# Performance work log

Measured on AMD Instinct MI355X. Metric: run time of the kernel, lower is better.

Reference implementation:

```python
import jax, jax.numpy as jnp
import numpy as np

SOS = 1  # letter2index['<sos>']
EOS = 0  # letter2index['<eos>'] (embedding padding_idx)

B, T, KV, E, H, V, L = 64, 2048, 128, 256, 512, 30, 256


def _lstm_cell(x, h, c, W_ih, W_hh, b_ih, b_hh):
    # PyTorch LSTMCell: gates ordered (i, f, g, o)
    gates = x @ W_ih.T + b_ih + h @ W_hh.T + b_hh
    i, f, g, o = jnp.split(gates, 4, axis=-1)
    c_new = jax.nn.sigmoid(f) * c + jax.nn.sigmoid(i) * jnp.tanh(g)
    h_new = jax.nn.sigmoid(o) * jnp.tanh(c_new)
    return h_new, c_new


def setup_inputs() -> dict:
    root = jax.random.key(0)
    ks = jax.random.split(root, 16)

    key = jax.random.normal(ks[0], (B, T, KV), dtype=jnp.float32)
    value = jax.random.normal(ks[1], (B, T, KV), dtype=jnp.float32)
    encoder_len = jax.random.randint(ks[2], (B,), 1, T + 1)
    y = jax.random.randint(ks[3], (B, L), 0, V)

    def w(k, shape, fan_in):
        return jax.random.normal(k, shape, dtype=jnp.float32) / np.sqrt(fan_in)

    emb_weight = w(ks[4], (V, E), E).at[EOS].set(0.0)  # padding_idx row zeroed
    in1 = E + KV
    W_ih1 = w(ks[5], (4 * H, in1), in1)
    W_hh1 = w(ks[6], (4 * H, H), H)
    b_ih1 = jnp.zeros((4 * H,), jnp.float32)
    b_hh1 = jnp.zeros((4 * H,), jnp.float32)
    W_ih2 = w(ks[7], (4 * KV, H), H)
    W_hh2 = w(ks[8], (4 * KV, KV), KV)
    b_ih2 = jnp.zeros((4 * KV,), jnp.float32)
    b_hh2 = jnp.zeros((4 * KV,), jnp.float32)
    out_bias = jnp.zeros((V,), jnp.float32)

    return dict(key=key, value=value, encoder_len=encoder_len, y=y,
                emb_weight=emb_weight,
                W_ih1=W_ih1, W_hh1=W_hh1, b_ih1=b_ih1, b_hh1=b_hh1,
                W_ih2=W_ih2, W_hh2=W_hh2, b_ih2=b_ih2, b_hh2=b_hh2,
                out_bias=out_bias)


def reference(key, value, encoder_len, y, emb_weight,
              W_ih1, W_hh1, b_ih1, b_hh1,
              W_ih2, W_hh2, b_ih2, b_hh2, out_bias):
    Bq, Tq, d_k = key.shape
    mask = jnp.arange(Tq)[None, :] >= encoder_len[:, None]  # (B, T) True = padded
    scale = 1.0 / np.sqrt(d_k).astype(np.float32)

    # Teacher forcing rate 1.0 in train mode: step i uses embed(SOS) at i=0,
    # embed(y[:, i-1]) afterwards.
    ids = jnp.concatenate([jnp.full((Bq, 1), SOS, dtype=y.dtype), y[:, :-1]], axis=1)
    embeds = emb_weight[ids]               # (B, L, E)
    embeds_t = jnp.swapaxes(embeds, 0, 1)  # (L, B, E)

    h_dim = W_hh1.shape[1]
    kv_dim = W_hh2.shape[1]
    init = (jnp.zeros((Bq, h_dim), key.dtype), jnp.zeros((Bq, h_dim), key.dtype),
            jnp.zeros((Bq, kv_dim), key.dtype), jnp.zeros((Bq, kv_dim), key.dtype),
            value.mean(axis=1))  # initial context

    def step(carry, char_embed):
        h1, c1, h2, c2, context = carry
        x = jnp.concatenate([char_embed, context], axis=1)
        h1, c1 = _lstm_cell(x, h1, c1, W_ih1, W_hh1, b_ih1, b_hh1)
        h2, c2 = _lstm_cell(h1, h2, c2, W_ih2, W_hh2, b_ih2, b_hh2)
        query = h2                                             # (B, KV)
        energy = jnp.einsum('bd,btd->bt', query, key) * scale  # (B, T)
        energy = jnp.where(mask, -1e9, energy)
        attn = jax.nn.softmax(energy, axis=1)
        ctx = jnp.einsum('bt,btd->bd', attn, value)            # (B, KV)
        logits = jnp.concatenate([query, ctx], axis=1) @ emb_weight.T + out_bias
        return (h1, c1, h2, c2, ctx), (logits, attn[0])

    _, (preds, attn_plot) = jax.lax.scan(step, init, embeds_t)
    predictions = jnp.swapaxes(preds, 0, 1)  # (B, L, V)
    return predictions, attn_plot            # attn_plot: (L, T), batch element 0
```

## Files before the change

### kernel.cpp

```cpp
#include <hip/hip_runtime.h>

#define NB 256
#define NT 1024

#define BB   64
#define TTS  2048
#define DKV  128
#define EEM  256
#define HH1  512
#define VVV  30
#define LLS  256
#define SOS_ID 1
#define SCALE_F 0.088388347648318447f

#define OFF_PM    0
#define OFF_PS    256
#define OFF_PCTX  512
#define OFF_WSE   33280
#define OFF_EMBT  35328
#define OFF_H1    68096
#define OFF_C1    133632
#define OFF_H2R   166400
#define OFF_H2T   182784
#define OFF_C2    199168
#define OFF_BAR   207360
#define OFF_KBF   212992
#define OFF_VBF   8601600
#define WS_NEED_BYTES 67960832ull
#define PRED_SZ   491520

struct Params {
  const float* key; const float* value;
  const int* enc_len; const int* y;
  const float* emb;
  const float* Wih1; const float* Whh1; const float* bih1; const float* bhh1;
  const float* Wih2; const float* Whh2; const float* bih2; const float* bhh2;
  const float* obias;
  float* out; float* ws;
};

struct SMEM {
  union {
    struct {
      float ctxT[8192];
      union { float wt[8192]; float red[8192]; } u;
    } a;
    struct { float wm[16]; float wS[16]; float wctx[2048]; } c;
  };
};

__device__ __forceinline__ float sigm(float x) { return 1.f / (1.f + __expf(-x)); }
__device__ __forceinline__ float tanh_f(float x) {
  float t = __expf(-2.f * fabsf(x));
  float r = (1.f - t) / (1.f + t);
  return x < 0.f ? -r : r;
}
__device__ __forceinline__ unsigned bfr(float f) {
  unsigned u = __float_as_uint(f);
  return (u + 0x7FFFu + ((u >> 16) & 1u)) >> 16;
}
__device__ __forceinline__ float b2f(unsigned short h) {
  return __uint_as_float(((unsigned)h) << 16);
}
__device__ __forceinline__ float blo(unsigned u) { return __uint_as_float(u << 16); }
__device__ __forceinline__ float bhi(unsigned u) { return __uint_as_float(u & 0xffff0000u); }

__device__ __forceinline__ void gbar(unsigned* base) {
  __syncthreads();
  if (threadIdx.x == 0) {
    __builtin_amdgcn_fence(__ATOMIC_RELEASE, "agent");
    unsigned* gen = base + 1056;
    unsigned g = __hip_atomic_load(gen, __ATOMIC_RELAXED, __HIP_MEMORY_SCOPE_AGENT);
    unsigned* gcnt = base + (blockIdx.x & 31) * 32;
    if (__hip_atomic_fetch_add(gcnt, 1u, __ATOMIC_RELAXED, __HIP_MEMORY_SCOPE_AGENT) == 7u) {
      unsigned* mcnt = base + 1024;
      if (__hip_atomic_fetch_add(mcnt, 1u, __ATOMIC_RELAXED, __HIP_MEMORY_SCOPE_AGENT) == 31u) {
        #pragma unroll
        for (int gg = 0; gg < 32; ++gg)
          __hip_atomic_store(base + gg * 32, 0u, __ATOMIC_RELAXED, __HIP_MEMORY_SCOPE_AGENT);
        __hip_atomic_store(mcnt, 0u, __ATOMIC_RELAXED, __HIP_MEMORY_SCOPE_AGENT);
        __hip_atomic_store(gen, g + 1u, __ATOMIC_RELEASE, __HIP_MEMORY_SCOPE_AGENT);
      }
    }
    int guard = 0;
    while (__hip_atomic_load(gen, __ATOMIC_RELAXED, __HIP_MEMORY_SCOPE_AGENT) == g) {
      __builtin_amdgcn_s_sleep(2);
      if (++guard > 50000000) break;
    }
    __builtin_amdgcn_fence(__ATOMIC_ACQUIRE, "agent");
  }
  __syncthreads();
}

__device__ __forceinline__ void mac8x4(float acc[8][4], const float* wt, int k, float4 x4) {
  float4 wa = *(const float4*)(wt + k*8);
  float4 wb = *(const float4*)(wt + k*8 + 4);
  float wr[8] = {wa.x, wa.y, wa.z, wa.w, wb.x, wb.y, wb.z, wb.w};
  float xr[4] = {x4.x, x4.y, x4.z, x4.w};
  #pragma unroll
  for (int r = 0; r < 8; ++r)
    #pragma unroll
    for (int c = 0; c < 4; ++c)
      acc[r][c] += wr[r] * xr[c];
}

__device__ __forceinline__ void gate_reduce_store(float acc[8][4], float* red, int tid) {
  #pragma unroll
  for (int r = 0; r < 8; ++r) {
    #pragma unroll
    for (int c = 0; c < 4; ++c) {
      float v = acc[r][c];
      v += __shfl_xor(v, 16);
      v += __shfl_xor(v, 32);
      acc[r][c] = v;
    }
  }
  int wv = tid >> 6, b0 = tid & 15;
  if ((tid & 63) < 16) {
    #pragma unroll
    for (int r = 0; r < 8; ++r)
      *(float4*)(red + wv*512 + r*64 + b0*4) =
        make_float4(acc[r][0], acc[r][1], acc[r][2], acc[r][3]);
  }
}

template<bool MEAN, bool BF16>
__device__ void phase_attn(const Params& p, const float* qrow,
                           const unsigned short* kbf, const unsigned short* vbf,
                           float* pm, float* pS, float* pctx, float* wsE,
                           SMEM* sm, int bj, int tid) {
  const int lane = tid & 63, w = tid >> 6;
  const int b = bj >> 2, s = bj & 3;
  const int len = MEAN ? TTS : p.enc_len[b];
  const int sub = lane & 15, grp = lane >> 4;
  const int q = 4*w + s;
  const int r0 = q*4 + grp;
  float m = -1e30f, S = 0.f;
  float ca[8] = {0.f,0.f,0.f,0.f,0.f,0.f,0.f,0.f};
  if constexpr (MEAN) {
    const float* vb = p.value + (size_t)b * TTS * DKV;
    #pragma unroll
    for (int j = 0; j < 8; ++j) {
      int t = r0 + 256*j;
      const float* vp = vb + (size_t)t * DKV + sub*8;
      float4 va = *(const float4*)vp;
      float4 vb4 = *(const float4*)(vp + 4);
      S += 1.f;
      ca[0]+=va.x;  ca[1]+=va.y;  ca[2]+=va.z;  ca[3]+=va.w;
      ca[4]+=vb4.x; ca[5]+=vb4.y; ca[6]+=vb4.z; ca[7]+=vb4.w;
    }
    m = 0.f;
  } else {
    int NJ = 0;
    if (len > q*4) { int nj = (len - q*4 + 255) >> 8; NJ = nj < 8 ? nj : 8; }
    if (NJ > 0) {
      float q8[8];
      {
        const float* qp = qrow + b*DKV + sub*8;
        float4 qa = *(const float4*)qp;
        float4 qb = *(const float4*)(qp + 4);
        q8[0]=qa.x; q8[1]=qa.y; q8[2]=qa.z; q8[3]=qa.w;
        q8[4]=qb.x; q8[5]=qb.y; q8[6]=qb.z; q8[7]=qb.w;
      }
      float e[8];
      #pragma unroll
      for (int j = 0; j < 8; ++j) e[j] = -1e30f;
      if constexpr (BF16) {
        const unsigned short* kb  = kbf + (size_t)(b*TTS)*DKV + sub*8;
        const unsigned short* vbp = vbf + (size_t)(b*TTS)*DKV + sub*8;
        uint4 kq[8], vq[8];
        #pragma unroll
        for (int j = 0; j < 8; ++j) {
          if (j < NJ) {
            int t = r0 + 256*j;
            int tc = t < len ? t : len - 1;
            kq[j] = *(const uint4*)(kb  + (size_t)tc * DKV);
            vq[j] = *(const uint4*)(vbp + (size_t)tc * DKV);
          }
        }
        __builtin_amdgcn_sched_barrier(0);
        #pragma unroll
        for (int j = 0; j < 8; ++j) {
          if (j < NJ) {
            float ep = blo(kq[j].x)*q8[0] + bhi(kq[j].x)*q8[1]
                     + blo(kq[j].y)*q8[2] + bhi(kq[j].y)*q8[3]
                     + blo(kq[j].z)*q8[4] + bhi(kq[j].z)*q8[5]
                     + blo(kq[j].w)*q8[6] + bhi(kq[j].w)*q8[7];
            ep += __shfl_xor(ep, 1); ep += __shfl_xor(ep, 2);
            ep += __shfl_xor(ep, 4); ep += __shfl_xor(ep, 8);
            int t = r0 + 256*j;
            e[j] = (t < len) ? ep * SCALE_F : -1e30f;
            if (b == 0 && sub == 0 && t < len) wsE[t] = e[j];
          }
        }
        m = fmaxf(fmaxf(fmaxf(e[0],e[1]), fmaxf(e[2],e[3])),
                  fmaxf(fmaxf(e[4],e[5]), fmaxf(e[6],e[7])));
        float pr[8];
        #pragma unroll
        for (int j = 0; j < 8; ++j) {
          pr[j] = (e[j] > -1e29f) ? __expf(e[j] - m) : 0.f;
          S += pr[j];
        }
        #pragma unroll
        for (int j = 0; j < 8; ++j) {
          if (j < NJ) {
            ca[0] += pr[j]*blo(vq[j].x); ca[1] += pr[j]*bhi(vq[j].x);
            ca[2] += pr[j]*blo(vq[j].y); ca[3] += pr[j]*bhi(vq[j].y);
            ca[4] += pr[j]*blo(vq[j].z); ca[5] += pr[j]*bhi(vq[j].z);
            ca[6] += pr[j]*blo(vq[j].w); ca[7] += pr[j]*bhi(vq[j].w);
          }
        }
      } else {
        #pragma unroll
        for (int j = 0; j < 8; ++j) {
          if (j < NJ) {
            int t = r0 + 256*j;
            int tc = t < len ? t : len - 1;
            const float* kp = p.key + (size_t)(b*TTS + tc)*DKV + sub*8;
            float4 ka = *(const float4*)kp;
            float4 kb2 = *(const float4*)(kp + 4);
            float ep = ka.x*q8[0] + ka.y*q8[1] + ka.z*q8[2] + ka.w*q8[3]
                     + kb2.x*q8[4] + kb2.y*q8[5] + kb2.z*q8[6] + kb2.w*q8[7];
            ep += __shfl_xor(ep, 1); ep += __shfl_xor(ep, 2);
            ep += __shfl_xor(ep, 4); ep += __shfl_xor(ep, 8);
            e[j] = (t < len) ? ep * SCALE_F : -1e30f;
            if (b == 0 && sub == 0 && t < len) wsE[t] = e[j];
          }
        }
        m = fmaxf(fmaxf(fmaxf(e[0],e[1]), fmaxf(e[2],e[3])),
                  fmaxf(fmaxf(e[4],e[5]), fmaxf(e[6],e[7])));
        float pr[8];
        #pragma unroll
        for (int j = 0; j < 8; ++j) {
          pr[j] = (e[j] > -1e29f) ? __expf(e[j] - m) : 0.f;
          S += pr[j];
        }
        #pragma unroll
        for (int j = 0; j < 8; ++j) {
          if (j < NJ) {
            int t = r0 + 256*j;
            int tc = t < len ? t : len - 1;
            const float* vp = p.value + (size_t)(b*TTS + tc)*DKV + sub*8;
            float4 va = *(const float4*)vp;
            float4 vb4 = *(const float4*)(vp + 4);
            ca[0] += pr[j]*va.x;  ca[1] += pr[j]*va.y;
            ca[2] += pr[j]*va.z;  ca[3] += pr[j]*va.w;
            ca[4] += pr[j]*vb4.x; ca[5] += pr[j]*vb4.y;
            ca[6] += pr[j]*vb4.z; ca[7] += pr[j]*vb4.w;
          }
        }
      }
    }
  }
  #pragma unroll
  for (int off = 16; off <= 32; off <<= 1) {
    float mo = __shfl_xor(m, off);
    float So = __shfl_xor(S, off);
    float M2 = fmaxf(m, mo);
    float a0 = __expf(m - M2), a1 = __expf(mo - M2);
    S = S*a0 + So*a1;
    #pragma unroll
    for (int d = 0; d < 8; ++d)
      ca[d] = ca[d]*a0 + __shfl_xor(ca[d], off)*a1;
    m = M2;
  }
  if (lane == 0) { sm->c.wm[w] = m; sm->c.wS[w] = S; }
  if (grp == 0) {
    *(float4*)(sm->c.wctx + w*DKV + sub*8)     = make_float4(ca[0],ca[1],ca[2],ca[3]);
    *(float4*)(sm->c.wctx + w*DKV + sub*8 + 4) = make_float4(ca[4],ca[5],ca[6],ca[7]);
  }
  __syncthreads();
  if (tid < DKV) {
    int d = tid;
    float M = -1e30f;
    #pragma unroll
    for (int ww = 0; ww < 16; ++ww) M = fmaxf(M, sm->c.wm[ww]);
    float Z = 0.f, acc2 = 0.f;
    #pragma unroll
    for (int ww = 0; ww < 16; ++ww) {
      float aw = __expf(sm->c.wm[ww] - M);
      Z += aw * sm->c.wS[ww];
      acc2 += aw * sm->c.wctx[ww*DKV + d];
    }
    pctx[d*256 + b*4 + s] = acc2;
    if (d == 0) { pm[b*4 + s] = M; pS[b*4 + s] = Z; }
  }
}

template<bool BF16>
__global__ void __launch_bounds__(NT, 4) decoder_kernel(Params p) {
  const int tid = threadIdx.x;
  const int bj = blockIdx.x;
  float* ws = p.ws;
  unsigned* bar = (unsigned*)(ws + OFF_BAR);
  float* pm = ws + OFF_PM;
  float* pS = ws + OFF_PS;
  float* pctx = ws + OFF_PCTX;
  float* wsE = ws + OFF_WSE;
  float* embT0 = ws + OFF_EMBT;
  float* embT1 = ws + OFF_EMBT + EEM*BB;
  float* h1b0 = ws + OFF_H1;
  float* h1b1 = ws + OFF_H1 + HH1*BB;
  float* c1 = ws + OFF_C1;
  float* h2r0 = ws + OFF_H2R;
  float* h2r1 = ws + OFF_H2R + BB*DKV;
  float* h2t0 = ws + OFF_H2T;
  float* h2t1 = ws + OFF_H2T + DKV*BB;
  float* c2 = ws + OFF_C2;
  unsigned short* kbf = (unsigned short*)(ws + OFF_KBF);
  unsigned short* vbf = (unsigned short*)(ws + OFF_VBF);

  __shared__ SMEM sm;

  float wr1[8] = {0,0,0,0,0,0,0,0};
  if (tid < 896) {
    #pragma unroll
    for (int r = 0; r < 8; ++r) {
      int grow = (r >> 1)*HH1 + 2*bj + (r & 1);
      wr1[r] = (tid < 384) ? p.Wih1[(size_t)grow*384 + tid]
                           : p.Whh1[(size_t)grow*HH1 + (tid - 384)];
    }
  }
  float wr2[8] = {0,0,0,0,0,0,0,0};
  if (bj < 64 && tid < 640) {
    #pragma unroll
    for (int r = 0; r < 8; ++r) {
      int grow = (r >> 1)*DKV + 2*bj + (r & 1);
      wr2[r] = (tid < 512) ? p.Wih2[(size_t)grow*HH1 + tid]
                           : p.Whh2[(size_t)grow*DKV + (tid - 512)];
    }
  }
  float bsum1 = 0.f, bsum2 = 0.f;
  if (tid < 512) {
    int r = tid >> 6;
    int g1 = (r >> 1)*HH1 + 2*bj + (r & 1);
    bsum1 = p.bih1[g1] + p.bhh1[g1];
    if (bj < 64) {
      int g2 = (r >> 1)*DKV + 2*bj + (r & 1);
      bsum2 = p.bih2[g2] + p.bhh2[g2];
    }
  }

  {
    int gid = bj*NT + tid;
    for (int idx = gid; idx < (OFF_BAR - OFF_H1); idx += NB*NT) ws[OFF_H1 + idx] = 0.f;
    for (int idx = gid; idx < EEM*BB; idx += NB*NT) {
      int k = idx >> 6, b = idx & 63;
      embT0[k*64 + b] = p.emb[SOS_ID*EEM + k];
    }
    if constexpr (BF16) {
      const int NG = (BB*TTS*DKV) / 8;
      for (int g = gid; g < NG; g += NB*NT) {
        const float4* src = (const float4*)p.key + (size_t)g*2;
        float4 a = src[0], bq = src[1];
        uint4 o;
        o.x = bfr(a.x)  | (bfr(a.y)  << 16);
        o.y = bfr(a.z)  | (bfr(a.w)  << 16);
        o.z = bfr(bq.x) | (bfr(bq.y) << 16);
        o.w = bfr(bq.z) | (bfr(bq.w) << 16);
        ((uint4*)kbf)[g] = o;
      }
      for (int g = gid; g < NG; g += NB*NT) {
        const float4* src = (const float4*)p.value + (size_t)g*2;
        float4 a = src[0], bq = src[1];
        uint4 o;
        o.x = bfr(a.x)  | (bfr(a.y)  << 16);
        o.y = bfr(a.z)  | (bfr(a.w)  << 16);
        o.z = bfr(bq.x) | (bfr(bq.y) << 16);
        o.w = bfr(bq.z) | (bfr(bq.w) << 16);
        ((uint4*)vbf)[g] = o;
      }
    }
    phase_attn<true, BF16>(p, nullptr, kbf, vbf, pm, pS, pctx, wsE, &sm, bj, tid);
  }
  gbar(bar);

  for (int i = 0; i <= LLS; ++i) {
    const int cur = i & 1;
    float* h1c = cur ? h1b1 : h1b0;
    const float* h1p = cur ? h1b0 : h1b1;
    float* h2rc = cur ? h2r1 : h2r0;
    const float* h2rp = cur ? h2r0 : h2r1;
    float* h2tc = cur ? h2t1 : h2t0;
    const float* h2tp = cur ? h2t0 : h2t1;
    const float* et = cur ? embT1 : embT0;
    float* etn = cur ? embT0 : embT1;

    {
      int b = tid & 63, dg = tid >> 6;
      float4 m4 = *(const float4*)(pm + b*4);
      float4 s4 = *(const float4*)(pS + b*4);
      float M = fmaxf(fmaxf(m4.x, m4.y), fmaxf(m4.z, m4.w));
      float a0 = __expf(m4.x - M), a1 = __expf(m4.y - M);
      float a2 = __expf(m4.z - M), a3 = __expf(m4.w - M);
      float Z = a0*s4.x + a1*s4.y + a2*s4.z + a3*s4.w;
      float iZ = 1.f / Z;
      a0 *= iZ; a1 *= iZ; a2 *= iZ; a3 *= iZ;
      #pragma unroll
      for (int jj = 0; jj < 8; ++jj) {
        int d = dg + jj*16;
        float4 c4 = *(const float4*)(pctx + d*256 + b*4);
        sm.a.ctxT[d*64 + b] = a0*c4.x + a1*c4.y + a2*c4.z + a3*c4.w;
      }
    }
    if (i < LLS && tid < 896) {
      *(float4*)(sm.a.u.wt + tid*8)     = make_float4(wr1[0], wr1[1], wr1[2], wr1[3]);
      *(float4*)(sm.a.u.wt + tid*8 + 4) = make_float4(wr1[4], wr1[5], wr1[6], wr1[7]);
    }
    __syncthreads();

    if (i < LLS) {
      {
        const int b0 = tid & 15, ks = tid >> 4;
        float acc[8][4];
        #pragma unroll
        for (int r = 0; r < 8; ++r) { acc[r][0]=0.f; acc[r][1]=0.f; acc[r][2]=0.f; acc[r][3]=0.f; }
        #pragma unroll
        for (int j = 0; j < 4; ++j) {
          int k = ks*4 + j;
          float4 x4 = *(const float4*)(et + k*64 + b0*4);
          mac8x4(acc, sm.a.u.wt, k, x4);
        }
        #pragma unroll
        for (int j = 0; j < 2; ++j) {
          int d = ks*2 + j;
          float4 x4 = *(const float4*)(sm.a.ctxT + d*64 + b0*4);
          mac8x4(acc, sm.a.u.wt, 256 + d, x4);
        }
        #pragma unroll
        for (int j = 0; j < 8; ++j) {
          int kk = ks*8 + j;
          float4 x4 = *(const float4*)(h1p + kk*64 + b0*4);
          mac8x4(acc, sm.a.u.wt, 384 + kk, x4);
        }
        __syncthreads();
        gate_reduce_store(acc, sm.a.u.red, tid);
      }
      __syncthreads();
      if (tid < 512) {
        int r = tid >> 6, b = tid & 63;
        float s = 0.f;
        #pragma unroll
        for (int w2 = 0; w2 < 16; ++w2) s += sm.a.u.red[w2*512 + r*64 + b];
        s += bsum1;
        sm.a.u.red[r*64 + b] = s;
      }
      __syncthreads();
      if (tid < 128) {
        int hh = tid >> 6, b = tid & 63;
        int h = 2*bj + hh;
        float gi = sm.a.u.red[(hh+0)*64 + b];
        float gf = sm.a.u.red[(hh+2)*64 + b];
        float gg = sm.a.u.red[(hh+4)*64 + b];
        float go = sm.a.u.red[(hh+6)*64 + b];
        float co = c1[h*64 + b];
        float cn = sigm(gf)*co + sigm(gi)*tanh_f(gg);
        float hn = sigm(go)*tanh_f(cn);
        c1[h*64 + b] = cn;
        h1c[h*64 + b] = hn;
      }
    }

    if (i >= 1) {
      if (tid >= 960) {
        int ln = tid - 960;
        int oi = bj*8 + (ln >> 3);
        int sub = ln & 7;
        if (oi < BB*VVV) {
          int b = oi / VVV, v = oi - b*VVV;
          float a = 0.f;
          if (sub < 4) {
            #pragma unroll 8
            for (int e0 = 0; e0 < 32; ++e0) {
              int e = sub*32 + e0;
              a += h2rp[b*DKV + e] * p.emb[v*EEM + e];
            }
          } else {
            #pragma unroll 8
            for (int e0 = 0; e0 < 32; ++e0) {
              int d = (sub - 4)*32 + e0;
              a += sm.a.ctxT[d*64 + b] * p.emb[v*EEM + 128 + d];
            }
          }
          a += __shfl_xor(a, 1); a += __shfl_xor(a, 2); a += __shfl_xor(a, 4);
          if (sub == 0) p.out[((size_t)b*LLS + (i-1))*VVV + v] = a + p.obias[v];
        }
      }
      if (tid >= 896 && tid < 904) {
        int t = bj*8 + (tid - 896);
        int len0 = p.enc_len[0];
        float v = 0.f;
        if (t < len0) {
          float m0 = pm[0], m1 = pm[1], m2 = pm[2], m3 = pm[3];
          float M = fmaxf(fmaxf(m0, m1), fmaxf(m2, m3));
          float Z = __expf(m0 - M)*pS[0] + __expf(m1 - M)*pS[1]
                  + __expf(m2 - M)*pS[2] + __expf(m3 - M)*pS[3];
          v = __expf(wsE[t] - M) / Z;
        }
        p.out[PRED_SZ + (size_t)(i-1)*TTS + t] = v;
      }
    }

    if (i == LLS) break;
    gbar(bar);

    if (bj < 64) {
      if (tid < 640) {
        *(float4*)(sm.a.u.wt + tid*8)     = make_float4(wr2[0], wr2[1], wr2[2], wr2[3]);
        *(float4*)(sm.a.u.wt + tid*8 + 4) = make_float4(wr2[4], wr2[5], wr2[6], wr2[7]);
      }
      __syncthreads();
      {
        const int b0 = tid & 15, ks = tid >> 4;
        float acc[8][4];
        #pragma unroll
        for (int r = 0; r < 8; ++r) { acc[r][0]=0.f; acc[r][1]=0.f; acc[r][2]=0.f; acc[r][3]=0.f; }
        #pragma unroll
        for (int j = 0; j < 8; ++j) {
          int k = ks*8 + j;
          float4 x4 = *(const float4*)(h1c + k*64 + b0*4);
          mac8x4(acc, sm.a.u.wt, k, x4);
        }
        #pragma unroll
        for (int j = 0; j < 2; ++j) {
          int d = ks*2 + j;
          float4 x4 = *(const float4*)(h2tp + d*64 + b0*4);
          mac8x4(acc, sm.a.u.wt, 512 + d, x4);
        }
        __syncthreads();
        gate_reduce_store(acc, sm.a.u.red, tid);
      }
      __syncthreads();
      if (tid < 512) {
        int r = tid >> 6, b = tid & 63;
        float s = 0.f;
        #pragma unroll
        for (int w2 = 0; w2 < 16; ++w2) s += sm.a.u.red[w2*512 + r*64 + b];
        s += bsum2;
        sm.a.u.red[r*64 + b] = s;
      }
      __syncthreads();
      if (tid < 128) {
        int hh = tid >> 6, b = tid & 63;
        int d2 = 2*bj + hh;
        float gi = sm.a.u.red[(hh+0)*64 + b];
        float gf = sm.a.u.red[(hh+2)*64 + b];
        float gg = sm.a.u.red[(hh+4)*64 + b];
        float go = sm.a.u.red[(hh+6)*64 + b];
        float co = c2[d2*64 + b];
        float cn = sigm(gf)*co + sigm(gi)*tanh_f(gg);
        float hn = sigm(go)*tanh_f(cn);
        c2[d2*64 + b] = cn;
        h2rc[b*DKV + d2] = hn;
        h2tc[d2*64 + b] = hn;
      }
    } else if (bj < 128) {
      int sn = i + 1;
      if (sn < LLS && tid < 256) {
        int idx = (bj - 64)*256 + tid;
        int k = idx >> 6, b = idx & 63;
        int id = p.y[b*LLS + sn - 1];
        etn[k*64 + b] = p.emb[(size_t)id*EEM + k];
      }
    }
    gbar(bar);

    phase_attn<false, BF16>(p, h2rc, kbf, vbf, pm, pS, pctx, wsE, &sm, bj, tid);
    gbar(bar);
  }
}

__global__ void init_bar_kernel(unsigned* bar) {
  int i = blockIdx.x * blockDim.x + threadIdx.x;
  if (i < 2048) bar[i] = 0u;
}

extern "C" void kernel_launch(void* const* d_in, const int* in_sizes, int n_in,
                              void* d_out, int out_size, void* d_ws, size_t ws_size,
                              hipStream_t stream) {
  Params prm;
  prm.key     = (const float*)d_in[0];
  prm.value   = (const float*)d_in[1];
  prm.enc_len = (const int*)d_in[2];
  prm.y       = (const int*)d_in[3];
  prm.emb     = (const float*)d_in[4];
  prm.Wih1    = (const float*)d_in[5];
  prm.Whh1    = (const float*)d_in[6];
  prm.bih1    = (const float*)d_in[7];
  prm.bhh1    = (const float*)d_in[8];
  prm.Wih2    = (const float*)d_in[9];
  prm.Whh2    = (const float*)d_in[10];
  prm.bih2    = (const float*)d_in[11];
  prm.bhh2    = (const float*)d_in[12];
  prm.obias   = (const float*)d_in[13];
  prm.out = (float*)d_out;
  prm.ws  = (float*)d_ws;

  unsigned* bar = (unsigned*)((float*)d_ws + OFF_BAR);
  init_bar_kernel<<<8, 256, 0, stream>>>(bar);

  void* args[] = { &prm };
  if (ws_size >= WS_NEED_BYTES) {
    hipError_t e = hipLaunchCooperativeKernel((const void*)decoder_kernel<true>,
                                              dim3(NB), dim3(NT), args, 0, stream);
    if (e != hipSuccess) decoder_kernel<true><<<dim3(NB), dim3(NT), 0, stream>>>(prm);
  } else {
    hipError_t e = hipLaunchCooperativeKernel((const void*)decoder_kernel<false>,
                                              dim3(NB), dim3(NT), args, 0, stream);
    if (e != hipSuccess) decoder_kernel<false><<<dim3(NB), dim3(NT), 0, stream>>>(prm);
  }
}
```

Baseline: 17.20 ms.

## Use per-group generation flags in grid barrier and remap attention block assignment

The grid barrier now has each group of eight blocks spin on its own generation flag, which is a monotonically increasing expected counter, instead of all blocks polling one shared word. The aim is to reduce contention on a single cache line. The attention phase remaps block-to-batch assignment so that consecutive blocks handle different batch rows, which spreads variable-length work across groups. It also splits the bf16 key and value loads into two batches to reduce register pressure. Barrier storage grows and the sleep interval is longer, which may add wake-up latency.

```diff
diff --git a/kernel.cpp b/kernel.cpp
--- a/kernel.cpp
+++ b/kernel.cpp
@@ -65,27 +65,30 @@
 __device__ __forceinline__ float blo(unsigned u) { return __uint_as_float(u << 16); }
 __device__ __forceinline__ float bhi(unsigned u) { return __uint_as_float(u & 0xffff0000u); }
 
-__device__ __forceinline__ void gbar(unsigned* base) {
+__device__ __forceinline__ void gbar(unsigned* base, unsigned expect) {
   __syncthreads();
   if (threadIdx.x == 0) {
     __builtin_amdgcn_fence(__ATOMIC_RELEASE, "agent");
-    unsigned* gen = base + 1056;
-    unsigned g = __hip_atomic_load(gen, __ATOMIC_RELAXED, __HIP_MEMORY_SCOPE_AGENT);
-    unsigned* gcnt = base + (blockIdx.x & 31) * 32;
+    const int grp = blockIdx.x >> 3;
+    unsigned* gcnt = base + grp * 32;
     if (__hip_atomic_fetch_add(gcnt, 1u, __ATOMIC_RELAXED, __HIP_MEMORY_SCOPE_AGENT) == 7u) {
       unsigned* mcnt = base + 1024;
       if (__hip_atomic_fetch_add(mcnt, 1u, __ATOMIC_RELAXED, __HIP_MEMORY_SCOPE_AGENT) == 31u) {
+        __hip_atomic_store(mcnt, 0u, __ATOMIC_RELAXED, __HIP_MEMORY_SCOPE_AGENT);
         #pragma unroll
         for (int gg = 0; gg < 32; ++gg)
           __hip_atomic_store(base + gg * 32, 0u, __ATOMIC_RELAXED, __HIP_MEMORY_SCOPE_AGENT);
-        __hip_atomic_store(mcnt, 0u, __ATOMIC_RELAXED, __HIP_MEMORY_SCOPE_AGENT);
-        __hip_atomic_store(gen, g + 1u, __ATOMIC_RELEASE, __HIP_MEMORY_SCOPE_AGENT);
-      }
-    }
+        __builtin_amdgcn_fence(__ATOMIC_RELEASE, "agent");
+        #pragma unroll
+        for (int gg = 0; gg < 32; ++gg)
+          __hip_atomic_store(base + 2048 + gg * 32, expect, __ATOMIC_RELAXED, __HIP_MEMORY_SCOPE_AGENT);
+      }
+    }
+    unsigned* mygen = base + 2048 + grp * 32;
     int guard = 0;
-    while (__hip_atomic_load(gen, __ATOMIC_RELAXED, __HIP_MEMORY_SCOPE_AGENT) == g) {
-      __builtin_amdgcn_s_sleep(2);
-      if (++guard > 50000000) break;
+    while ((int)(__hip_atomic_load(mygen, __ATOMIC_RELAXED, __HIP_MEMORY_SCOPE_AGENT) - expect) < 0) {
+      __builtin_amdgcn_s_sleep(8);
+      if (++guard > 10000000) break;
     }
     __builtin_amdgcn_fence(__ATOMIC_ACQUIRE, "agent");
   }
@@ -130,7 +133,8 @@
                            float* pm, float* pS, float* pctx, float* wsE,
                            SMEM* sm, int bj, int tid) {
   const int lane = tid & 63, w = tid >> 6;
-  const int b = bj >> 2, s = bj & 3;
+  const int b = ((bj & 7) << 3) | ((bj >> 3) & 7);
+  const int s = bj >> 6;
   const int len = MEAN ? TTS : p.enc_len[b];
   const int sub = lane & 15, grp = lane >> 4;
   const int q = 4*w + s;
@@ -150,105 +154,97 @@
       ca[4]+=vb4.x; ca[5]+=vb4.y; ca[6]+=vb4.z; ca[7]+=vb4.w;
     }
     m = 0.f;
-  } else {
-    int NJ = 0;
-    if (len > q*4) { int nj = (len - q*4 + 255) >> 8; NJ = nj < 8 ? nj : 8; }
-    if (NJ > 0) {
-      float q8[8];
-      {
-        const float* qp = qrow + b*DKV + sub*8;
-        float4 qa = *(const float4*)qp;
-        float4 qb = *(const float4*)(qp + 4);
-        q8[0]=qa.x; q8[1]=qa.y; q8[2]=qa.z; q8[3]=qa.w;
-        q8[4]=qb.x; q8[5]=qb.y; q8[6]=qb.z; q8[7]=qb.w;
-      }
-      float e[8];
-      #pragma unroll
-      for (int j = 0; j < 8; ++j) e[j] = -1e30f;
-      if constexpr (BF16) {
-        const unsigned short* kb  = kbf + (size_t)(b*TTS)*DKV + sub*8;
-        const unsigned short* vbp = vbf + (size_t)(b*TTS)*DKV + sub*8;
-        uint4 kq[8], vq[8];
-        #pragma unroll
-        for (int j = 0; j < 8; ++j) {
-          if (j < NJ) {
-            int t = r0 + 256*j;
-            int tc = t < len ? t : len - 1;
-            kq[j] = *(const uint4*)(kb  + (size_t)tc * DKV);
-            vq[j] = *(const uint4*)(vbp + (size_t)tc * DKV);
-          }
-        }
-        __builtin_amdgcn_sched_barrier(0);
-        #pragma unroll
-        for (int j = 0; j < 8; ++j) {
-          if (j < NJ) {
-            float ep = blo(kq[j].x)*q8[0] + bhi(kq[j].x)*q8[1]
-                     + blo(kq[j].y)*q8[2] + bhi(kq[j].y)*q8[3]
-                     + blo(kq[j].z)*q8[4] + bhi(kq[j].z)*q8[5]
-                     + blo(kq[j].w)*q8[6] + bhi(kq[j].w)*q8[7];
-            ep += __shfl_xor(ep, 1); ep += __shfl_xor(ep, 2);
-            ep += __shfl_xor(ep, 4); ep += __shfl_xor(ep, 8);
-            int t = r0 + 256*j;
-            e[j] = (t < len) ? ep * SCALE_F : -1e30f;
-            if (b == 0 && sub == 0 && t < len) wsE[t] = e[j];
-          }
-        }
-        m = fmaxf(fmaxf(fmaxf(e[0],e[1]), fmaxf(e[2],e[3])),
-                  fmaxf(fmaxf(e[4],e[5]), fmaxf(e[6],e[7])));
-        float pr[8];
-        #pragma unroll
-        for (int j = 0; j < 8; ++j) {
-          pr[j] = (e[j] > -1e29f) ? __expf(e[j] - m) : 0.f;
-          S += pr[j];
-        }
-        #pragma unroll
-        for (int j = 0; j < 8; ++j) {
-          if (j < NJ) {
-            ca[0] += pr[j]*blo(vq[j].x); ca[1] += pr[j]*bhi(vq[j].x);
-            ca[2] += pr[j]*blo(vq[j].y); ca[3] += pr[j]*bhi(vq[j].y);
-            ca[4] += pr[j]*blo(vq[j].z); ca[5] += pr[j]*bhi(vq[j].z);
-            ca[6] += pr[j]*blo(vq[j].w); ca[7] += pr[j]*bhi(vq[j].w);
-          }
-        }
-      } else {
-        #pragma unroll
-        for (int j = 0; j < 8; ++j) {
-          if (j < NJ) {
-            int t = r0 + 256*j;
-            int tc = t < len ? t : len - 1;
-            const float* kp = p.key + (size_t)(b*TTS + tc)*DKV + sub*8;
-            float4 ka = *(const float4*)kp;
-            float4 kb2 = *(const float4*)(kp + 4);
-            float ep = ka.x*q8[0] + ka.y*q8[1] + ka.z*q8[2] + ka.w*q8[3]
-                     + kb2.x*q8[4] + kb2.y*q8[5] + kb2.z*q8[6] + kb2.w*q8[7];
-            ep += __shfl_xor(ep, 1); ep += __shfl_xor(ep, 2);
-            ep += __shfl_xor(ep, 4); ep += __shfl_xor(ep, 8);
-            e[j] = (t < len) ? ep * SCALE_F : -1e30f;
-            if (b == 0 && sub == 0 && t < len) wsE[t] = e[j];
-          }
-        }
-        m = fmaxf(fmaxf(fmaxf(e[0],e[1]), fmaxf(e[2],e[3])),
-                  fmaxf(fmaxf(e[4],e[5]), fmaxf(e[6],e[7])));
-        float pr[8];
-        #pragma unroll
-        for (int j = 0; j < 8; ++j) {
-          pr[j] = (e[j] > -1e29f) ? __expf(e[j] - m) : 0.f;
-          S += pr[j];
-        }
-        #pragma unroll
-        for (int j = 0; j < 8; ++j) {
-          if (j < NJ) {
-            int t = r0 + 256*j;
-            int tc = t < len ? t : len - 1;
-            const float* vp = p.value + (size_t)(b*TTS + tc)*DKV + sub*8;
-            float4 va = *(const float4*)vp;
-            float4 vb4 = *(const float4*)(vp + 4);
-            ca[0] += pr[j]*va.x;  ca[1] += pr[j]*va.y;
-            ca[2] += pr[j]*va.z;  ca[3] += pr[j]*va.w;
-            ca[4] += pr[j]*vb4.x; ca[5] += pr[j]*vb4.y;
-            ca[6] += pr[j]*vb4.z; ca[7] += pr[j]*vb4.w;
-          }
-        }
+  } else if (len > q*4) {
+    float q8[8];
+    {
+      const float* qp = qrow + b*DKV + sub*8;
+      float4 qa = *(const float4*)qp;
+      float4 qb = *(const float4*)(qp + 4);
+      q8[0]=qa.x; q8[1]=qa.y; q8[2]=qa.z; q8[3]=qa.w;
+      q8[4]=qb.x; q8[5]=qb.y; q8[6]=qb.z; q8[7]=qb.w;
+    }
+    float e[8];
+    if constexpr (BF16) {
+      const unsigned short* kb  = kbf + (size_t)(b*TTS)*DKV + sub*8;
+      const unsigned short* vbp = vbf + (size_t)(b*TTS)*DKV + sub*8;
+      int tcs[8];
+      #pragma unroll
+      for (int j = 0; j < 8; ++j) {
+        int t = r0 + 256*j;
+        tcs[j] = t < len ? t : len - 1;
+      }
+      uint4 kq[8];
+      #pragma unroll
+      for (int j = 0; j < 8; ++j) kq[j] = *(const uint4*)(kb + (size_t)tcs[j]*DKV);
+      __builtin_amdgcn_sched_barrier(0);
+      #pragma unroll
+      for (int j = 0; j < 8; ++j) {
+        float ep = blo(kq[j].x)*q8[0] + bhi(kq[j].x)*q8[1]
+                 + blo(kq[j].y)*q8[2] + bhi(kq[j].y)*q8[3]
+                 + blo(kq[j].z)*q8[4] + bhi(kq[j].z)*q8[5]
+                 + blo(kq[j].w)*q8[6] + bhi(kq[j].w)*q8[7];
+        ep += __shfl_xor(ep, 1); ep += __shfl_xor(ep, 2);
+        ep += __shfl_xor(ep, 4); ep += __shfl_xor(ep, 8);
+        int t = r0 + 256*j;
+        e[j] = (t < len) ? ep * SCALE_F : -1e30f;
+        if (b == 0 && sub == 0 && t < len) wsE[t] = e[j];
+      }
+      m = fmaxf(fmaxf(fmaxf(e[0],e[1]), fmaxf(e[2],e[3])),
+                fmaxf(fmaxf(e[4],e[5]), fmaxf(e[6],e[7])));
+      float pr[8];
+      #pragma unroll
+      for (int j = 0; j < 8; ++j) {
+        pr[j] = (e[j] > -1e29f) ? __expf(e[j] - m) : 0.f;
+        S += pr[j];
+      }
+      uint4 vq[8];
+      #pragma unroll
+      for (int j = 0; j < 8; ++j) vq[j] = *(const uint4*)(vbp + (size_t)tcs[j]*DKV);
+      __builtin_amdgcn_sched_barrier(0);
+      #pragma unroll
+      for (int j = 0; j < 8; ++j) {
+        ca[0] += pr[j]*blo(vq[j].x); ca[1] += pr[j]*bhi(vq[j].x);
+        ca[2] += pr[j]*blo(vq[j].y); ca[3] += pr[j]*bhi(vq[j].y);
+        ca[4] += pr[j]*blo(vq[j].z); ca[5] += pr[j]*bhi(vq[j].z);
+        ca[6] += pr[j]*blo(vq[j].w); ca[7] += pr[j]*bhi(vq[j].w);
+      }
+    } else {
+      int tcs[8];
+      #pragma unroll
+      for (int j = 0; j < 8; ++j) {
+        int t = r0 + 256*j;
+        tcs[j] = t < len ? t : len - 1;
+      }
+      #pragma unroll
+      for (int j = 0; j < 8; ++j) {
+        const float* kp = p.key + (size_t)(b*TTS + tcs[j])*DKV + sub*8;
+        float4 ka = *(const float4*)kp;
+        float4 kb2 = *(const float4*)(kp + 4);
+        float ep = ka.x*q8[0] + ka.y*q8[1] + ka.z*q8[2] + ka.w*q8[3]
+                 + kb2.x*q8[4] + kb2.y*q8[5] + kb2.z*q8[6] + kb2.w*q8[7];
+        ep += __shfl_xor(ep, 1); ep += __shfl_xor(ep, 2);
+        ep += __shfl_xor(ep, 4); ep += __shfl_xor(ep, 8);
+        int t = r0 + 256*j;
+        e[j] = (t < len) ? ep * SCALE_F : -1e30f;
+        if (b == 0 && sub == 0 && t < len) wsE[t] = e[j];
+      }
+      m = fmaxf(fmaxf(fmaxf(e[0],e[1]), fmaxf(e[2],e[3])),
+                fmaxf(fmaxf(e[4],e[5]), fmaxf(e[6],e[7])));
+      float pr[8];
+      #pragma unroll
+      for (int j = 0; j < 8; ++j) {
+        pr[j] = (e[j] > -1e29f) ? __expf(e[j] - m) : 0.f;
+        S += pr[j];
+      }
+      #pragma unroll
+      for (int j = 0; j < 8; ++j) {
+        const float* vp = p.value + (size_t)(b*TTS + tcs[j])*DKV + sub*8;
+        float4 va = *(const float4*)vp;
+        float4 vb4 = *(const float4*)(vp + 4);
+        ca[0] += pr[j]*va.x;  ca[1] += pr[j]*va.y;
+        ca[2] += pr[j]*va.z;  ca[3] += pr[j]*va.w;
+        ca[4] += pr[j]*vb4.x; ca[5] += pr[j]*vb4.y;
+        ca[6] += pr[j]*vb4.z; ca[7] += pr[j]*vb4.w;
       }
     }
   }
@@ -309,6 +305,7 @@
   float* c2 = ws + OFF_C2;
   unsigned short* kbf = (unsigned short*)(ws + OFF_KBF);
   unsigned short* vbf = (unsigned short*)(ws + OFF_VBF);
+  unsigned genc = 0;
 
   __shared__ SMEM sm;
 
@@ -373,7 +370,7 @@
     }
     phase_attn<true, BF16>(p, nullptr, kbf, vbf, pm, pS, pctx, wsE, &sm, bj, tid);
   }
-  gbar(bar);
+  gbar(bar, ++genc);
 
   for (int i = 0; i <= LLS; ++i) {
     const int cur = i & 1;
@@ -502,7 +499,7 @@
     }
 
     if (i == LLS) break;
-    gbar(bar);
+    gbar(bar, ++genc);
 
     if (bj < 64) {
       if (tid < 640) {
@@ -563,16 +560,16 @@
         etn[k*64 + b] = p.emb[(size_t)id*EEM + k];
       }
     }
-    gbar(bar);
+    gbar(bar, ++genc);
 
     phase_attn<false, BF16>(p, h2rc, kbf, vbf, pm, pS, pctx, wsE, &sm, bj, tid);
-    gbar(bar);
+    gbar(bar, ++genc);
   }
 }
 
 __global__ void init_bar_kernel(unsigned* bar) {
   int i = blockIdx.x * blockDim.x + threadIdx.x;
-  if (i < 2048) bar[i] = 0u;
+  if (i < 4096) bar[i] = 0u;
 }
 
 extern "C" void kernel_launch(void* const* d_in, const int* in_sizes, int n_in,
@@ -597,7 +594,7 @@
   prm.ws  = (float*)d_ws;
 
   unsigned* bar = (unsigned*)((float*)d_ws + OFF_BAR);
-  init_bar_kernel<<<8, 256, 0, stream>>>(bar);
+  init_bar_kernel<<<16, 256, 0, stream>>>(bar);
 
   void* args[] = { &prm };
   if (ws_size >= WS_NEED_BYTES) {
```

Measured after the change: 18.51 ms. 1.08x slower.
